# Performance work log

Measured on AMD Instinct MI355X. Metric: run time of the kernel, lower is better.

The kernel has to match this reference:

```python
import jax, jax.numpy as jnp
import numpy as np

EPS = 1e-5
GROUPS = 8


def _bn(x, gamma, beta, mean, var, axis):
    # inference-mode batchnorm along `axis`
    shape = [1] * x.ndim
    shape[axis] = -1
    scale = gamma.reshape(shape) * jax.lax.rsqrt(var.reshape(shape) + EPS)
    return (x - mean.reshape(shape)) * scale + beta.reshape(shape)


def setup_inputs() -> dict:
    key = jax.random.key(0)
    ks = jax.random.split(key, 16)
    N, C, H, W = 8, 128, 128, 128
    out_planes = 128
    x = jax.random.normal(ks[0], (N, C, H, W), jnp.float32)
    w_qkv = jax.random.normal(ks[1], (2 * out_planes, C), jnp.float32) * np.float32(np.sqrt(1.0 / C))

    def bn_params(k, c):
        k1, k2, k3, k4 = jax.random.split(k, 4)
        gamma = jax.random.uniform(k1, (c,), jnp.float32, 0.5, 1.5)
        beta = jax.random.normal(k2, (c,), jnp.float32) * 0.1
        mean = jax.random.normal(k3, (c,), jnp.float32) * 0.1
        var = jax.random.uniform(k4, (c,), jnp.float32, 0.5, 1.5)
        return gamma, beta, mean, var

    qg, qb, qm, qv = bn_params(ks[2], 2 * out_planes)
    sg, sb, sm, sv = bn_params(ks[3], GROUPS)
    og, ob, om, ov = bn_params(ks[4], out_planes)
    return {
        'x': x, 'w_qkv': w_qkv,
        'qkv_gamma': qg, 'qkv_beta': qb, 'qkv_mean': qm, 'qkv_var': qv,
        'sim_gamma': sg, 'sim_beta': sb, 'sim_mean': sm, 'sim_var': sv,
        'out_gamma': og, 'out_beta': ob, 'out_mean': om, 'out_var': ov,
    }


def reference(x, w_qkv, qkv_gamma, qkv_beta, qkv_mean, qkv_var,
              sim_gamma, sim_beta, sim_mean, sim_var,
              out_gamma, out_beta, out_mean, out_var):
    N, C, H, W = x.shape
    groups = GROUPS
    out_planes = w_qkv.shape[0] // 2
    gp = out_planes // groups  # group_planes

    # width=False: (N,C,H,W) -> (N,W,C,H) -> (N*W, C, H)
    xb = jnp.transpose(x, (0, 3, 1, 2)).reshape(N * W, C, H)
    # conv1x1 qkv transform + BN1d over channels
    qkv = jnp.einsum('bci,oc->boi', xb, w_qkv)
    qkv = _bn(qkv, qkv_gamma, qkv_beta, qkv_mean, qkv_var, axis=1)
    qkv = qkv.reshape(N * W, groups, 2 * gp, H)
    q = qkv[:, :, : gp // 2]          # (NW, g, gp/2, H)
    k = qkv[:, :, gp // 2: gp]        # (NW, g, gp/2, H)
    v = qkv[:, :, gp:]                # (NW, g, gp,   H)

    qk = jnp.einsum('bgci,bgcj->bgij', q, k)  # (NW, g, H, H)
    sim = _bn(qk, sim_gamma, sim_beta, sim_mean, sim_var, axis=1)
    sim = jax.nn.softmax(sim, axis=3)

    sv = jnp.einsum('bgij,bgcj->bgci', sim, v)  # (NW, g, gp, H)
    sv = sv.reshape(N * W, out_planes, H)
    out = _bn(sv, out_gamma, out_beta, out_mean, out_var, axis=1)
    out = out.reshape(N, W, out_planes, H)
    # permute(0,2,3,1): (N, out_planes, H, W)
    return jnp.transpose(out, (0, 2, 3, 1))
```

## Files before the change

kernel.cpp:

```cpp
#include <hip/hip_runtime.h>
#include <math.h>

#define EPS 1e-5f

typedef _Float16 half4 __attribute__((ext_vector_type(4)));
typedef _Float16 half8 __attribute__((ext_vector_type(8)));
typedef float floatx4 __attribute__((ext_vector_type(4)));

__global__ void transpose_cvt_k(const float* __restrict__ x, _Float16* __restrict__ xt2) {
  __shared__ float tile[64][65];
  int nh = blockIdx.x;
  int n = nh >> 7, h = nh & 127;
  int c0 = blockIdx.y * 64, w0 = blockIdx.z * 64;
  const float* src = x + (size_t)n * 2097152 + (size_t)h * 128;
  _Float16* dst = xt2 + (size_t)n * 2097152 + (size_t)h * 128;
  int lane = threadIdx.x & 63;
  int tr = threadIdx.x >> 6;
#pragma unroll
  for (int rr = tr; rr < 64; rr += 4)
    tile[rr][lane] = src[(size_t)(c0 + rr) * 16384 + w0 + lane];
  __syncthreads();
#pragma unroll
  for (int cc = tr; cc < 64; cc += 4)
    dst[(size_t)(w0 + cc) * 16384 + c0 + lane] = (_Float16)tile[lane][cc];
}

__global__ void __launch_bounds__(256, 2) qkv_mfma_kernel(
    const _Float16* __restrict__ xt2, const float* __restrict__ wq,
    const float* __restrict__ qg, const float* __restrict__ qb,
    const float* __restrict__ qm, const float* __restrict__ qv,
    _Float16* __restrict__ qkv16) {
  __shared__ _Float16 As[128][136];
  __shared__ _Float16 Bs[128][136];
  __shared__ float scs[128];
  __shared__ float bis[128];
  int b = blockIdx.x >> 1;
  int oh = blockIdx.x & 1;
  int t = threadIdx.x;

  {
    const float* wbase = wq + (size_t)oh * 128 * 128;
#pragma unroll
    for (int idx = t; idx < 4096; idx += 256) {
      int o = idx >> 5, c4 = (idx & 31) * 4;
      float4 v = *(const float4*)(wbase + (size_t)o * 128 + c4);
      As[o][c4 + 0] = (_Float16)v.x;
      As[o][c4 + 1] = (_Float16)v.y;
      As[o][c4 + 2] = (_Float16)v.z;
      As[o][c4 + 3] = (_Float16)v.w;
    }
  }
  {
    const _Float16* xb = xt2 + (size_t)b * 16384;
#pragma unroll
    for (int idx = t; idx < 2048; idx += 256) {
      int i = idx >> 4, c8 = (idx & 15) * 8;
      half8 v = *(const half8*)(xb + (size_t)i * 128 + c8);
      *(half8*)(&Bs[i][c8]) = v;
    }
  }
  if (t < 128) {
    int o = oh * 128 + t;
    float sc = qg[o] * rsqrtf(qv[o] + EPS);
    scs[t] = sc;
    bis[t] = qb[o] - qm[o] * sc;
  }
  __syncthreads();

  int wv = t >> 6;
  int lane = t & 63;
  int m0 = (wv & 1) * 64;
  int n0 = (wv >> 1) * 64;
  int lrow = lane & 15;
  int quad = lane >> 4;

  floatx4 acc[4][4];
#pragma unroll
  for (int mt = 0; mt < 4; mt++)
#pragma unroll
    for (int nt = 0; nt < 4; nt++)
#pragma unroll
      for (int r = 0; r < 4; r++) acc[mt][nt][r] = 0.f;

#pragma unroll
  for (int k0 = 0; k0 < 128; k0 += 32) {
    half8 af[4], bf[4];
#pragma unroll
    for (int mt = 0; mt < 4; mt++)
      af[mt] = *(const half8*)(&As[m0 + mt * 16 + lrow][k0 + quad * 8]);
#pragma unroll
    for (int nt = 0; nt < 4; nt++)
      bf[nt] = *(const half8*)(&Bs[n0 + nt * 16 + lrow][k0 + quad * 8]);
#pragma unroll
    for (int mt = 0; mt < 4; mt++)
#pragma unroll
      for (int nt = 0; nt < 4; nt++)
        acc[mt][nt] = __builtin_amdgcn_mfma_f32_16x16x32_f16(af[mt], bf[nt], acc[mt][nt], 0, 0, 0);
  }

  _Float16* outb = qkv16 + (size_t)b * 32768 + (size_t)oh * 16384;
#pragma unroll
  for (int mt = 0; mt < 4; mt++) {
#pragma unroll
    for (int r = 0; r < 4; r++) {
      int o_l = m0 + mt * 16 + quad * 4 + r;
      float sc = scs[o_l];
      float bi = bis[o_l];
#pragma unroll
      for (int nt = 0; nt < 4; nt++) {
        int i = n0 + nt * 16 + lrow;
        outb[(size_t)o_l * 128 + i] = (_Float16)fmaf(acc[mt][nt][r], sc, bi);
      }
    }
  }
}

__global__ void __launch_bounds__(64) attn_mfma_kernel(
    const _Float16* __restrict__ qkv16,
    const float* __restrict__ sg, const float* __restrict__ sb,
    const float* __restrict__ sm, const float* __restrict__ svv,
    const float* __restrict__ og, const float* __restrict__ ob,
    const float* __restrict__ om, const float* __restrict__ ov,
    _Float16* __restrict__ svout) {
  __shared__ _Float16 plds[16 * 136];
  int bg = blockIdx.x;
  int b = bg >> 3, g = bg & 7;
  int t = threadIdx.x;
  int n = t & 15;
  int q4 = t >> 4;

  const _Float16* base = qkv16 + (size_t)b * 32768 + (size_t)g * 4096;
  const _Float16* kb = base + 1024;
  const _Float16* vb = base + 2048;

  half8 kf[8];
#pragma unroll
  for (int jt = 0; jt < 8; jt++)
#pragma unroll
    for (int jj = 0; jj < 8; jj++)
      kf[jt][jj] = kb[jj * 128 + jt * 16 + n];

  half8 vf[4];
#pragma unroll
  for (int ks = 0; ks < 4; ks++)
    vf[ks] = *(const half8*)(vb + (size_t)n * 128 + ks * 32 + q4 * 8);

  float s_scale = sg[g] * rsqrtf(svv[g] + EPS);
  float sc4 = s_scale * 0.25f;
  float s_bias = sb[g] - sm[g] * s_scale;

  float osc[4], obi[4];
#pragma unroll
  for (int r = 0; r < 4; r++) {
    int oc = g * 16 + q4 * 4 + r;
    float s0 = og[oc] * rsqrtf(ov[oc] + EPS);
    osc[r] = s0;
    obi[r] = ob[oc] - om[oc] * s0;
  }

  for (int st8 = 0; st8 < 8; st8++) {
    half8 qf;
#pragma unroll
    for (int jj = 0; jj < 8; jj++)
      qf[jj] = base[jj * 128 + st8 * 16 + n];

    floatx4 stt[8];
#pragma unroll
    for (int jt = 0; jt < 8; jt++) {
      floatx4 z = {0.f, 0.f, 0.f, 0.f};
      stt[jt] = __builtin_amdgcn_mfma_f32_16x16x32_f16(kf[jt], qf, z, 0, 0, 0);
    }

    float mx = -1e30f;
#pragma unroll
    for (int jt = 0; jt < 8; jt++)
#pragma unroll
      for (int r = 0; r < 4; r++) {
        stt[jt][r] = fmaf(stt[jt][r], sc4, s_bias);
        mx = fmaxf(mx, stt[jt][r]);
      }
    mx = fmaxf(mx, __shfl_xor(mx, 16));
    mx = fmaxf(mx, __shfl_xor(mx, 32));

    float ls = 0.f;
#pragma unroll
    for (int jt = 0; jt < 8; jt++)
#pragma unroll
      for (int r = 0; r < 4; r++) {
        float e = __expf(stt[jt][r] - mx);
        stt[jt][r] = e;
        ls += e;
      }
    ls += __shfl_xor(ls, 16);
    ls += __shfl_xor(ls, 32);

#pragma unroll
    for (int jt = 0; jt < 8; jt++) {
      half4 h;
      h[0] = (_Float16)stt[jt][0];
      h[1] = (_Float16)stt[jt][1];
      h[2] = (_Float16)stt[jt][2];
      h[3] = (_Float16)stt[jt][3];
      *(half4*)(&plds[n * 136 + jt * 16 + q4 * 4]) = h;
    }

    floatx4 oacc = {0.f, 0.f, 0.f, 0.f};
#pragma unroll
    for (int ks = 0; ks < 4; ks++) {
      half8 pf = *(const half8*)(&plds[n * 136 + ks * 32 + q4 * 8]);
      oacc = __builtin_amdgcn_mfma_f32_16x16x32_f16(vf[ks], pf, oacc, 0, 0, 0);
    }

    float invl = 1.f / ls;
    _Float16* outp = svout + ((size_t)b * 128 + g * 16 + q4 * 4) * 128 + st8 * 16 + n;
#pragma unroll
    for (int r = 0; r < 4; r++)
      outp[(size_t)r * 128] = (_Float16)fmaf(oacc[r] * invl, osc[r], obi[r]);
  }
}

__global__ void transpose_h2f_k(const _Float16* __restrict__ in, float* __restrict__ out,
                                int R, int C) {
  __shared__ float tile[64][65];
  int nblk = blockIdx.x;
  int r0 = blockIdx.y * 64;
  int c0 = blockIdx.z * 64;
  const _Float16* src = in + (size_t)nblk * R * C;
  float* dst = out + (size_t)nblk * R * C;
  int lane = threadIdx.x & 63;
  int tr = threadIdx.x >> 6;
#pragma unroll
  for (int rr = tr; rr < 64; rr += 4)
    tile[rr][lane] = (float)src[(size_t)(r0 + rr) * C + c0 + lane];
  __syncthreads();
#pragma unroll
  for (int cc = tr; cc < 64; cc += 4)
    dst[(size_t)(c0 + cc) * R + r0 + lane] = tile[lane][cc];
}

extern "C" void kernel_launch(void* const* d_in, const int* in_sizes, int n_in,
                              void* d_out, int out_size, void* d_ws, size_t ws_size,
                              hipStream_t stream) {
  const float* x  = (const float*)d_in[0];
  const float* wq = (const float*)d_in[1];
  const float* qg = (const float*)d_in[2];
  const float* qb = (const float*)d_in[3];
  const float* qm = (const float*)d_in[4];
  const float* qv = (const float*)d_in[5];
  const float* sg = (const float*)d_in[6];
  const float* sb = (const float*)d_in[7];
  const float* sm = (const float*)d_in[8];
  const float* sv = (const float*)d_in[9];
  const float* og = (const float*)d_in[10];
  const float* ob = (const float*)d_in[11];
  const float* om = (const float*)d_in[12];
  const float* ov = (const float*)d_in[13];
  float* out = (float*)d_out;

  _Float16* qkv16 = (_Float16*)d_ws;
  _Float16* xt2 = qkv16 + (size_t)1024 * 256 * 128;
  _Float16* svh = xt2 + (size_t)1024 * 128 * 128;

  transpose_cvt_k<<<dim3(1024, 2, 2), 256, 0, stream>>>(x, xt2);
  qkv_mfma_kernel<<<2048, 256, 0, stream>>>(xt2, wq, qg, qb, qm, qv, qkv16);
  attn_mfma_kernel<<<8192, 64, 0, stream>>>(qkv16, sg, sb, sm, sv, og, ob, om, ov, svh);
  transpose_h2f_k<<<dim3(8, 2, 256), 256, 0, stream>>>(svh, out, 128, 16384);
}
```

Measured before the change: 262.2 us.

## Fuse output transpose into attention kernel via LDS staging across batch rows

```diff
diff --git a/kernel.cpp b/kernel.cpp
--- a/kernel.cpp
+++ b/kernel.cpp
@@ -44,10 +44,12 @@
     for (int idx = t; idx < 4096; idx += 256) {
       int o = idx >> 5, c4 = (idx & 31) * 4;
       float4 v = *(const float4*)(wbase + (size_t)o * 128 + c4);
-      As[o][c4 + 0] = (_Float16)v.x;
-      As[o][c4 + 1] = (_Float16)v.y;
-      As[o][c4 + 2] = (_Float16)v.z;
-      As[o][c4 + 3] = (_Float16)v.w;
+      half4 hv;
+      hv[0] = (_Float16)v.x;
+      hv[1] = (_Float16)v.y;
+      hv[2] = (_Float16)v.z;
+      hv[3] = (_Float16)v.w;
+      *(half4*)(&As[o][c4]) = hv;
     }
   }
   {
@@ -115,39 +117,29 @@
   }
 }
 
-__global__ void __launch_bounds__(64) attn_mfma_kernel(
+__global__ void __launch_bounds__(512, 4) attn_mfma_fused_kernel(
     const _Float16* __restrict__ qkv16,
     const float* __restrict__ sg, const float* __restrict__ sb,
     const float* __restrict__ sm, const float* __restrict__ svv,
-    const float* __restrict__ og, const float* __restrict__ ob,
+    const float* __restrict__ og, const float* __restrict__ obt,
     const float* __restrict__ om, const float* __restrict__ ov,
-    _Float16* __restrict__ svout) {
-  __shared__ _Float16 plds[16 * 136];
-  int bg = blockIdx.x;
-  int b = bg >> 3, g = bg & 7;
+    float* __restrict__ out) {
+  __shared__ _Float16 olds[16][128][8];
+  __shared__ _Float16 plds[8][2176];
+  int bid = blockIdx.x;
+  int nn = bid >> 7;
+  int g = (bid >> 4) & 7;
+  int wt = bid & 15;
   int t = threadIdx.x;
-  int n = t & 15;
-  int q4 = t >> 4;
-
-  const _Float16* base = qkv16 + (size_t)b * 32768 + (size_t)g * 4096;
-  const _Float16* kb = base + 1024;
-  const _Float16* vb = base + 2048;
-
-  half8 kf[8];
-#pragma unroll
-  for (int jt = 0; jt < 8; jt++)
-#pragma unroll
-    for (int jj = 0; jj < 8; jj++)
-      kf[jt][jj] = kb[jj * 128 + jt * 16 + n];
-
-  half8 vf[4];
-#pragma unroll
-  for (int ks = 0; ks < 4; ks++)
-    vf[ks] = *(const half8*)(vb + (size_t)n * 128 + ks * 32 + q4 * 8);
+  int wv = t >> 6;
+  int lane = t & 63;
+  int ln = lane & 15;
+  int q4 = lane >> 4;
 
   float s_scale = sg[g] * rsqrtf(svv[g] + EPS);
-  float sc4 = s_scale * 0.25f;
-  float s_bias = sb[g] - sm[g] * s_scale;
+  float sc4 = s_scale * 0.25f * 1.44269504f;
+  (void)sb;
+  (void)sm;
 
   float osc[4], obi[4];
 #pragma unroll
@@ -155,14 +147,32 @@
     int oc = g * 16 + q4 * 4 + r;
     float s0 = og[oc] * rsqrtf(ov[oc] + EPS);
     osc[r] = s0;
-    obi[r] = ob[oc] - om[oc] * s0;
-  }
+    obi[r] = obt[oc] - om[oc] * s0;
+  }
+
+  _Float16* pw = &plds[wv][0];
+  int b = nn * 128 + wt * 8 + wv;
+  const _Float16* base = qkv16 + (size_t)b * 32768 + (size_t)g * 4096;
+  const _Float16* kb = base + 1024;
+  const _Float16* vb = base + 2048;
+
+  half8 kf[8];
+#pragma unroll
+  for (int jt = 0; jt < 8; jt++)
+#pragma unroll
+    for (int jj = 0; jj < 8; jj++)
+      kf[jt][jj] = kb[jj * 128 + jt * 16 + ln];
+
+  half8 vf[4];
+#pragma unroll
+  for (int ks = 0; ks < 4; ks++)
+    vf[ks] = *(const half8*)(vb + (size_t)ln * 128 + ks * 32 + q4 * 8);
 
   for (int st8 = 0; st8 < 8; st8++) {
     half8 qf;
 #pragma unroll
     for (int jj = 0; jj < 8; jj++)
-      qf[jj] = base[jj * 128 + st8 * 16 + n];
+      qf[jj] = base[jj * 128 + st8 * 16 + ln];
 
     floatx4 stt[8];
 #pragma unroll
@@ -176,7 +186,7 @@
     for (int jt = 0; jt < 8; jt++)
 #pragma unroll
       for (int r = 0; r < 4; r++) {
-        stt[jt][r] = fmaf(stt[jt][r], sc4, s_bias);
+        stt[jt][r] *= sc4;
         mx = fmaxf(mx, stt[jt][r]);
       }
     mx = fmaxf(mx, __shfl_xor(mx, 16));
@@ -187,7 +197,7 @@
     for (int jt = 0; jt < 8; jt++)
 #pragma unroll
       for (int r = 0; r < 4; r++) {
-        float e = __expf(stt[jt][r] - mx);
+        float e = exp2f(stt[jt][r] - mx);
         stt[jt][r] = e;
         ls += e;
       }
@@ -201,41 +211,38 @@
       h[1] = (_Float16)stt[jt][1];
       h[2] = (_Float16)stt[jt][2];
       h[3] = (_Float16)stt[jt][3];
-      *(half4*)(&plds[n * 136 + jt * 16 + q4 * 4]) = h;
+      *(half4*)(&pw[ln * 136 + jt * 16 + q4 * 4]) = h;
     }
 
     floatx4 oacc = {0.f, 0.f, 0.f, 0.f};
 #pragma unroll
     for (int ks = 0; ks < 4; ks++) {
-      half8 pf = *(const half8*)(&plds[n * 136 + ks * 32 + q4 * 8]);
+      half8 pf = *(const half8*)(&pw[ln * 136 + ks * 32 + q4 * 8]);
       oacc = __builtin_amdgcn_mfma_f32_16x16x32_f16(vf[ks], pf, oacc, 0, 0, 0);
     }
 
     float invl = 1.f / ls;
-    _Float16* outp = svout + ((size_t)b * 128 + g * 16 + q4 * 4) * 128 + st8 * 16 + n;
 #pragma unroll
     for (int r = 0; r < 4; r++)
-      outp[(size_t)r * 128] = (_Float16)fmaf(oacc[r] * invl, osc[r], obi[r]);
-  }
-}
-
-__global__ void transpose_h2f_k(const _Float16* __restrict__ in, float* __restrict__ out,
-                                int R, int C) {
-  __shared__ float tile[64][65];
-  int nblk = blockIdx.x;
-  int r0 = blockIdx.y * 64;
-  int c0 = blockIdx.z * 64;
-  const _Float16* src = in + (size_t)nblk * R * C;
-  float* dst = out + (size_t)nblk * R * C;
-  int lane = threadIdx.x & 63;
-  int tr = threadIdx.x >> 6;
-#pragma unroll
-  for (int rr = tr; rr < 64; rr += 4)
-    tile[rr][lane] = (float)src[(size_t)(r0 + rr) * C + c0 + lane];
+      olds[q4 * 4 + r][st8 * 16 + ln][wv] = (_Float16)fmaf(oacc[r] * invl, osc[r], obi[r]);
+  }
+
   __syncthreads();
-#pragma unroll
-  for (int cc = tr; cc < 64; cc += 4)
-    dst[(size_t)(c0 + cc) * R + r0 + lane] = tile[lane][cc];
+
+  float* outp = out + ((size_t)nn * 128 + g * 16) * 16384 + wt * 8;
+#pragma unroll
+  for (int idx = t; idx < 4096; idx += 512) {
+    int w4 = idx & 1;
+    int h = (idx >> 1) & 127;
+    int c = idx >> 8;
+    half4 v = *(const half4*)(&olds[c][h][w4 * 4]);
+    float4 f;
+    f.x = (float)v[0];
+    f.y = (float)v[1];
+    f.z = (float)v[2];
+    f.w = (float)v[3];
+    *(float4*)(outp + (size_t)c * 16384 + (size_t)h * 128 + w4 * 4) = f;
+  }
 }
 
 extern "C" void kernel_launch(void* const* d_in, const int* in_sizes, int n_in,
@@ -259,10 +266,9 @@
 
   _Float16* qkv16 = (_Float16*)d_ws;
   _Float16* xt2 = qkv16 + (size_t)1024 * 256 * 128;
-  _Float16* svh = xt2 + (size_t)1024 * 128 * 128;
 
   transpose_cvt_k<<<dim3(1024, 2, 2), 256, 0, stream>>>(x, xt2);
   qkv_mfma_kernel<<<2048, 256, 0, stream>>>(xt2, wq, qg, qb, qm, qv, qkv16);
-  attn_mfma_kernel<<<8192, 64, 0, stream>>>(qkv16, sg, sb, sm, sv, og, ob, om, ov, svh);
-  transpose_h2f_k<<<dim3(8, 2, 256), 256, 0, stream>>>(svh, out, 128, 16384);
-}
+  attn_mfma_fused_kernel<<<1024, 512, 0, stream>>>(qkv16, sg, sb, sm, sv,
+                                                   og, ob, om, ov, out);
+}
```

Result: no change. 262.3 us (+0.0%).
